# Kernel optimization log

Measured on AMD Instinct MI355X. Metric: run time of the kernel, lower is better.

Reference implementation:

```python
import jax, jax.numpy as jnp
import numpy as np

N = 2048          # num nodes == in_channels (f1 = graphs[0].shape[0])
F_IN = 2048       # node feature dim
G1 = 10           # ChebConv out channels
E = 65536         # num edges (avg degree 32)
NUM_CLASSES = 10  # fc1 output


def setup_inputs() -> dict:
    key = jax.random.key(0)
    ks = jax.random.split(key, 6)
    x = jax.random.normal(ks[0], (N, F_IN), dtype=jnp.float32)
    edge_index = jax.random.randint(ks[1], (2, E), 0, N)
    # ChebConv weights: one [F_IN, G1] matrix per Chebyshev order (K=2), glorot-ish init
    s = float(1.0 / np.sqrt(F_IN))
    W0 = jax.random.uniform(ks[2], (F_IN, G1), jnp.float32, -s, s)
    W1 = jax.random.uniform(ks[3], (F_IN, G1), jnp.float32, -s, s)
    b = jnp.zeros((G1,), jnp.float32)
    sf = float(1.0 / np.sqrt(G1))
    Wf = jax.random.uniform(ks[4], (G1, NUM_CLASSES), jnp.float32, -sf, sf)
    bf = jax.random.uniform(ks[5], (NUM_CLASSES,), jnp.float32, -sf, sf)
    return {"x": x, "edge_index": edge_index, "W0": W0, "W1": W1, "b": b, "Wf": Wf, "bf": bf}


def _cheb_edge_weights(edge_index):
    # PyG ChebConv default: sym-normalized Laplacian scaled with lambda_max=2.0.
    # L_hat = 2*L/lambda_max - I = -D^{-1/2} A D^{-1/2}  (zero diagonal).
    row, col = edge_index[0], edge_index[1]
    deg = jax.ops.segment_sum(jnp.ones((E,), jnp.float32), row, num_segments=N)
    dis = jnp.where(deg > 0, jax.lax.rsqrt(jnp.maximum(deg, 1.0)), 0.0)
    return -dis[row] * dis[col]


def reference(x, edge_index, W0, W1, b, Wf, bf):
    row, col = edge_index[0], edge_index[1]
    w = _cheb_edge_weights(edge_index)
    # Tx_0 = x ; Tx_1 = L_hat @ x via gather (source=row) + scatter-add (target=col)
    Tx1 = jax.ops.segment_sum(w[:, None] * x[row], col, num_segments=N)  # [N, F_IN]
    h = x @ W0 + Tx1 @ W1 + b                                            # ChebConv, K=2
    h = jax.nn.relu(h)
    logits = h @ Wf + bf                                                 # fc1
    return jax.nn.log_softmax(logits, axis=1)
```

## Files before the change

kernel.cpp:

```cpp
#include <hip/hip_runtime.h>

#define N_NODES 2048
#define F_IN    2048
#define G1      10
#define NCLS    10
#define NEDGE   65536
#define JC      32
#define JPER    64
#define ROWS    128
#define HS      128
#define ZS      64

__device__ float g_p[JC * 20 * N_NODES];
__device__ int   g_degp[HS * N_NODES];
__device__ float g_y[N_NODES * 20];
__device__ float g_dis[N_NODES];
__device__ float g_zp[2 * ZS * N_NODES * 5];

__global__ __launch_bounds__(256) void k_gemm(const float* __restrict__ x,
                                              const float* __restrict__ W0,
                                              const float* __restrict__ W1,
                                              const int* __restrict__ ei) {
    __shared__ __align__(16) float smem[ROWS * 65];
    const int tid = threadIdx.x;
    const int bx  = blockIdx.x;
    int jc   = bx & (JC - 1);
    int rb   = bx >> 5;
    int j0   = jc * JPER;
    int row0 = rb * ROWS;

    #pragma unroll
    for (int rep = 0; rep < 8; ++rep) {
        int idx = rep * 256 + tid;
        int r = idx >> 4, c4 = idx & 15;
        float4 v = *(const float4*)(x + (size_t)(row0 + r) * F_IN + j0 + c4 * 4);
        float* d = smem + r * 65 + c4 * 4;
        d[0] = v.x; d[1] = v.y; d[2] = v.z; d[3] = v.w;
    }
    __syncthreads();

    int ri = tid & (ROWS - 1);
    int kg = tid >> 7;
    const float* Wm = kg ? W1 : W0;
    float acc[G1];
    #pragma unroll
    for (int k = 0; k < G1; ++k) acc[k] = 0.f;
    const float* xr = smem + ri * 65;
    #pragma unroll
    for (int j = 0; j < JPER; ++j) {
        float xu = xr[j];
        const float* wr = Wm + (size_t)(j0 + j) * G1;
        #pragma unroll
        for (int k = 0; k < G1; ++k) acc[k] += xu * wr[k];
    }
    int row = row0 + ri;
    #pragma unroll
    for (int k = 0; k < G1; ++k)
        g_p[((size_t)jc * 20 + kg * 10 + k) * N_NODES + row] = acc[k];

    if (bx < HS) {
        __syncthreads();
        int* h = (int*)smem;
        #pragma unroll
        for (int t = tid; t < N_NODES; t += 256) h[t] = 0;
        __syncthreads();
        int base = bx * (NEDGE / HS);
        atomicAdd(&h[ei[base + tid]], 1);
        atomicAdd(&h[ei[base + 256 + tid]], 1);
        __syncthreads();
        #pragma unroll
        for (int t = tid; t < N_NODES; t += 256)
            g_degp[bx * N_NODES + t] = h[t];
    }
}

__global__ __launch_bounds__(256) void k_reduce() {
    int t   = blockIdx.x * 256 + threadIdx.x;
    int k   = t >> 11;
    int row = t & (N_NODES - 1);
    float s = 0.f;
    #pragma unroll 8
    for (int jc = 0; jc < JC; ++jc)
        s += g_p[((size_t)jc * 20 + k) * N_NODES + row];
    g_y[row * 20 + k] = s;
    if (t < N_NODES) {
        int d = 0;
        #pragma unroll 16
        for (int sl = 0; sl < HS; ++sl) d += g_degp[sl * N_NODES + t];
        g_dis[t] = (d > 0) ? rsqrtf((float)d) : 0.f;
    }
}

__global__ __launch_bounds__(256) void k_scatter(const int* __restrict__ ei) {
    __shared__ float zl[N_NODES * 5];
    int khalf  = blockIdx.x >> 6;
    int bslice = blockIdx.x & (ZS - 1);
    float4* zl4 = (float4*)zl;
    #pragma unroll
    for (int t = threadIdx.x; t < N_NODES * 5 / 4; t += 256)
        zl4[t] = make_float4(0.f, 0.f, 0.f, 0.f);
    __syncthreads();
    int base = bslice * (NEDGE / ZS);
    #pragma unroll
    for (int u = 0; u < NEDGE / ZS / 256; ++u) {
        int e = base + u * 256 + threadIdx.x;
        int r = ei[e], c = ei[NEDGE + e];
        float w = -g_dis[r] * g_dis[c];
        const float* y1 = g_y + r * 20 + 10 + khalf * 5;
        float* zz = zl + c * 5;
        #pragma unroll
        for (int kk = 0; kk < 5; ++kk) atomicAdd(&zz[kk], w * y1[kk]);
    }
    __syncthreads();
    float4* dst = (float4*)(g_zp + ((size_t)khalf * ZS + bslice) * (N_NODES * 5));
    #pragma unroll
    for (int t = threadIdx.x; t < N_NODES * 5 / 4; t += 256) dst[t] = zl4[t];
}

__global__ __launch_bounds__(320) void k_final(const float* __restrict__ b,
                                               const float* __restrict__ Wf,
                                               const float* __restrict__ bfv,
                                               float* __restrict__ out) {
    __shared__ float sh[320];
    int tid = threadIdx.x;
    int t = blockIdx.x * 320 + tid;
    int i = t / 10, k = t - i * 10;
    int khalf = k / 5, kk = k - khalf * 5;
    float s = 0.f;
    #pragma unroll 16
    for (int sl = 0; sl < ZS; ++sl)
        s += g_zp[((size_t)khalf * ZS + sl) * (N_NODES * 5) + i * 5 + kk];
    sh[tid] = fmaxf(g_y[i * 20 + k] + s + b[k], 0.f);
    __syncthreads();
    if (tid < 32) {
        int node = blockIdx.x * 32 + tid;
        const float* h = sh + tid * 10;
        float lo[NCLS];
        #pragma unroll
        for (int c = 0; c < NCLS; ++c) lo[c] = bfv[c];
        #pragma unroll
        for (int kq = 0; kq < G1; ++kq) {
            float hk = h[kq];
            #pragma unroll
            for (int c = 0; c < NCLS; ++c) lo[c] += hk * Wf[kq * NCLS + c];
        }
        float m = lo[0];
        #pragma unroll
        for (int c = 1; c < NCLS; ++c) m = fmaxf(m, lo[c]);
        float sum = 0.f;
        #pragma unroll
        for (int c = 0; c < NCLS; ++c) sum += expf(lo[c] - m);
        float ls = logf(sum);
        #pragma unroll
        for (int c = 0; c < NCLS; ++c) out[node * NCLS + c] = lo[c] - m - ls;
    }
}

extern "C" void kernel_launch(void* const* d_in, const int* in_sizes, int n_in,
                              void* d_out, int out_size, void* d_ws, size_t ws_size,
                              hipStream_t stream) {
    const float* x   = (const float*)d_in[0];
    const int*   ei  = (const int*)d_in[1];
    const float* W0  = (const float*)d_in[2];
    const float* W1  = (const float*)d_in[3];
    const float* b   = (const float*)d_in[4];
    const float* Wf  = (const float*)d_in[5];
    const float* bfv = (const float*)d_in[6];
    float* out = (float*)d_out;

    k_gemm<<<dim3(JC * (N_NODES / ROWS)), 256, 0, stream>>>(x, W0, W1, ei);
    k_reduce<<<(N_NODES * 20) / 256, 256, 0, stream>>>();
    k_scatter<<<2 * ZS, 256, 0, stream>>>(ei);
    k_final<<<N_NODES / 32, 320, 0, stream>>>(b, Wf, bfv, out);
}
```

Baseline: 110.8 us.

## Drop reduce kernel using global atomics for GEMM partials and degree counts

```diff
diff --git a/kernel.cpp b/kernel.cpp
--- a/kernel.cpp
+++ b/kernel.cpp
@@ -5,90 +5,56 @@
 #define G1      10
 #define NCLS    10
 #define NEDGE   65536
-#define JC      32
-#define JPER    64
-#define ROWS    128
-#define HS      128
+#define JC      8
+#define JPER    256
+#define ROWS    64
 #define ZS      64
 
-__device__ float g_p[JC * 20 * N_NODES];
-__device__ int   g_degp[HS * N_NODES];
 __device__ float g_y[N_NODES * 20];
-__device__ float g_dis[N_NODES];
+__device__ int   g_deg[N_NODES];
 __device__ float g_zp[2 * ZS * N_NODES * 5];
 
 __global__ __launch_bounds__(256) void k_gemm(const float* __restrict__ x,
                                               const float* __restrict__ W0,
                                               const float* __restrict__ W1,
                                               const int* __restrict__ ei) {
-    __shared__ __align__(16) float smem[ROWS * 65];
+    __shared__ __align__(16) float smem[ROWS * 257];
     const int tid = threadIdx.x;
     const int bx  = blockIdx.x;
     int jc   = bx & (JC - 1);
-    int rb   = bx >> 5;
+    int rb   = bx >> 3;
     int j0   = jc * JPER;
     int row0 = rb * ROWS;
 
     #pragma unroll
-    for (int rep = 0; rep < 8; ++rep) {
+    for (int rep = 0; rep < 16; ++rep) {
         int idx = rep * 256 + tid;
-        int r = idx >> 4, c4 = idx & 15;
+        int r = idx >> 6, c4 = idx & 63;
         float4 v = *(const float4*)(x + (size_t)(row0 + r) * F_IN + j0 + c4 * 4);
-        float* d = smem + r * 65 + c4 * 4;
+        float* d = smem + r * 257 + c4 * 4;
         d[0] = v.x; d[1] = v.y; d[2] = v.z; d[3] = v.w;
     }
+    atomicAdd(&g_deg[ei[bx * 256 + tid]], 1);
     __syncthreads();
 
-    int ri = tid & (ROWS - 1);
-    int kg = tid >> 7;
-    const float* Wm = kg ? W1 : W0;
-    float acc[G1];
-    #pragma unroll
-    for (int k = 0; k < G1; ++k) acc[k] = 0.f;
-    const float* xr = smem + ri * 65;
-    #pragma unroll
+    int ri   = tid & (ROWS - 1);
+    int kg   = tid >> 6;
+    int mat  = kg >> 1;
+    int half = kg & 1;
+    const float* Wm = mat ? W1 : W0;
+    float acc[5] = {0.f, 0.f, 0.f, 0.f, 0.f};
+    const float* xr = smem + ri * 257;
+    #pragma unroll 8
     for (int j = 0; j < JPER; ++j) {
         float xu = xr[j];
-        const float* wr = Wm + (size_t)(j0 + j) * G1;
+        const float* wr = Wm + (size_t)(j0 + j) * G1 + half * 5;
         #pragma unroll
-        for (int k = 0; k < G1; ++k) acc[k] += xu * wr[k];
+        for (int k = 0; k < 5; ++k) acc[k] += xu * wr[k];
     }
     int row = row0 + ri;
     #pragma unroll
-    for (int k = 0; k < G1; ++k)
-        g_p[((size_t)jc * 20 + kg * 10 + k) * N_NODES + row] = acc[k];
-
-    if (bx < HS) {
-        __syncthreads();
-        int* h = (int*)smem;
-        #pragma unroll
-        for (int t = tid; t < N_NODES; t += 256) h[t] = 0;
-        __syncthreads();
-        int base = bx * (NEDGE / HS);
-        atomicAdd(&h[ei[base + tid]], 1);
-        atomicAdd(&h[ei[base + 256 + tid]], 1);
-        __syncthreads();
-        #pragma unroll
-        for (int t = tid; t < N_NODES; t += 256)
-            g_degp[bx * N_NODES + t] = h[t];
-    }
-}
-
-__global__ __launch_bounds__(256) void k_reduce() {
-    int t   = blockIdx.x * 256 + threadIdx.x;
-    int k   = t >> 11;
-    int row = t & (N_NODES - 1);
-    float s = 0.f;
-    #pragma unroll 8
-    for (int jc = 0; jc < JC; ++jc)
-        s += g_p[((size_t)jc * 20 + k) * N_NODES + row];
-    g_y[row * 20 + k] = s;
-    if (t < N_NODES) {
-        int d = 0;
-        #pragma unroll 16
-        for (int sl = 0; sl < HS; ++sl) d += g_degp[sl * N_NODES + t];
-        g_dis[t] = (d > 0) ? rsqrtf((float)d) : 0.f;
-    }
+    for (int k = 0; k < 5; ++k)
+        atomicAdd(&g_y[row * 20 + mat * 10 + half * 5 + k], acc[k]);
 }
 
 __global__ __launch_bounds__(256) void k_scatter(const int* __restrict__ ei) {
@@ -105,7 +71,9 @@
     for (int u = 0; u < NEDGE / ZS / 256; ++u) {
         int e = base + u * 256 + threadIdx.x;
         int r = ei[e], c = ei[NEDGE + e];
-        float w = -g_dis[r] * g_dis[c];
+        int dr = g_deg[r], dc = g_deg[c];
+        float w = -(dr > 0 ? rsqrtf((float)dr) : 0.f) *
+                   (dc > 0 ? rsqrtf((float)dc) : 0.f);
         const float* y1 = g_y + r * 20 + 10 + khalf * 5;
         float* zz = zl + c * 5;
         #pragma unroll
@@ -131,6 +99,9 @@
     for (int sl = 0; sl < ZS; ++sl)
         s += g_zp[((size_t)khalf * ZS + sl) * (N_NODES * 5) + i * 5 + kk];
     sh[tid] = fmaxf(g_y[i * 20 + k] + s + b[k], 0.f);
+    g_y[i * 20 + k]      = 0.f;
+    g_y[i * 20 + 10 + k] = 0.f;
+    if (t < N_NODES) g_deg[t] = 0;
     __syncthreads();
     if (tid < 32) {
         int node = blockIdx.x * 32 + tid;
@@ -169,7 +140,6 @@
     float* out = (float*)d_out;
 
     k_gemm<<<dim3(JC * (N_NODES / ROWS)), 256, 0, stream>>>(x, W0, W1, ei);
-    k_reduce<<<(N_NODES * 20) / 256, 256, 0, stream>>>();
     k_scatter<<<2 * ZS, 256, 0, stream>>>(ei);
     k_final<<<N_NODES / 32, 320, 0, stream>>>(b, Wf, bfv, out);
 }
```

Measured after the change: 122.1 us. +10.2%, slower.
